# Performance work log

Hardware: AMD Instinct MI355X
Metric: run time of the kernel (lower is better)

The kernel has to match this reference:

```python
import jax, jax.numpy as jnp
import numpy as np
import math

B, S, D_MODEL, H, D_LATENT = 2, 2048, 2048, 16, 512
D_HEAD = D_MODEL // H


def setup_inputs() -> dict:
    key = jax.random.key(0)
    ks = jax.random.split(key, 6)
    s = lambda fan: 1.0 / math.sqrt(fan)
    return {
        "x": jax.random.normal(ks[0], (B, S, D_MODEL), dtype=jnp.float32),
        "W_q": jax.random.normal(ks[1], (D_MODEL, D_MODEL), dtype=jnp.float32) * s(D_MODEL),
        "W_down_kv": jax.random.normal(ks[2], (D_LATENT, D_MODEL), dtype=jnp.float32) * s(D_MODEL),
        "W_up_k": jax.random.normal(ks[3], (H, D_HEAD, D_LATENT), dtype=jnp.float32) * s(D_LATENT),
        "W_up_v": jax.random.normal(ks[4], (H, D_HEAD, D_LATENT), dtype=jnp.float32) * s(D_LATENT),
        "W_o": jax.random.normal(ks[5], (D_MODEL, D_MODEL), dtype=jnp.float32) * s(D_MODEL),
    }


def reference(x, W_q, W_down_kv, W_up_k, W_up_v, W_o):
    b, s_len, d_model = x.shape
    # Q: (B, H, S, Dh)
    Q = (x @ W_q.T).reshape(b, s_len, H, D_HEAD).transpose(0, 2, 1, 3)
    # latent KV: (B, S, d_latent)
    C_kv = x @ W_down_kv.T
    # per-head up-projections fused into one einsum: (B, H, S, Dh)
    K = jnp.einsum("bsl,hdl->bhsd", C_kv, W_up_k)
    V = jnp.einsum("bsl,hdl->bhsd", C_kv, W_up_v)
    scores = jnp.einsum("bhsd,bhtd->bhst", Q, K) / math.sqrt(D_HEAD)
    attn = jax.nn.softmax(scores, axis=-1)  # dropout p=0 / eval -> identity
    out = jnp.einsum("bhst,bhtd->bhsd", attn, V)
    out = out.transpose(0, 2, 1, 3).reshape(b, s_len, H * D_HEAD)
    return out @ W_o.T
```

## Files before the change

kernel.cpp:

```cpp
#include <hip/hip_runtime.h>
#include <hip/hip_bf16.h>

typedef __hip_bfloat16 bf16;
typedef __attribute__((ext_vector_type(8))) short short8v;
typedef __attribute__((ext_vector_type(4))) short short4v;
typedef __attribute__((ext_vector_type(4))) float f32x4;
typedef __attribute__((ext_vector_type(16))) float f32x16;
typedef __attribute__((ext_vector_type(4))) unsigned int uint4v;
typedef unsigned int u32;

#define MFMA_16x16x32(a, b, c) __builtin_amdgcn_mfma_f32_16x16x32_bf16((a), (b), (c), 0, 0, 0)
#define MFMA_32x32x16(a, b, c) __builtin_amdgcn_mfma_f32_32x32x16_bf16((a), (b), (c), 0, 0, 0)

constexpr int Bc = 2, Sc = 2048, DMc = 2048, Hc = 16, DLc = 512, DHc = 128;

__device__ __forceinline__ void gload_lds16(const bf16* g, void* lds) {
  __builtin_amdgcn_global_load_lds(
      (const __attribute__((address_space(1))) void*)g,
      (__attribute__((address_space(3))) void*)lds, 16, 0, 0);
}

__device__ __forceinline__ unsigned short bf16bits(float f) {
  return __builtin_bit_cast(unsigned short, __float2bfloat16(f));
}

struct CvtArgs {
  const float* src[6];
  bf16* dst[6];
  unsigned int cum[6];
  unsigned int total4;
};

__global__ __launch_bounds__(256) void cvt_all_kernel(CvtArgs a)
{
  unsigned int i = blockIdx.x * 256 + threadIdx.x;
  const unsigned int stride = gridDim.x * 256;
  for (; i < a.total4; i += stride) {
    int s = 0;
#pragma unroll
    for (int k = 1; k < 6; ++k) s += (i >= a.cum[k]) ? 1 : 0;
    unsigned int off = (i - a.cum[s]) * 4;
    float4 v = *(const float4*)(a.src[s] + off);
    short4v p;
    p[0] = (short)bf16bits(v.x);
    p[1] = (short)bf16bits(v.y);
    p[2] = (short)bf16bits(v.z);
    p[3] = (short)bf16bits(v.w);
    *(short4v*)(a.dst[s] + off) = p;
  }
}

template<int EPI>
__device__ __forceinline__ void gemm_tile_128(
    const bf16* __restrict__ A, const bf16* __restrict__ BT, void* __restrict__ Cv,
    int K, int ldc, int row0, int col0, bf16* As, bf16* Bs)
{
  const int tid = threadIdx.x;
  const int lane = tid & 63, wid = tid >> 6;
  const int wr = wid >> 1, wc = wid & 1;

  f32x4 acc[4][4] = {};

  const int srow = tid >> 2;
  const int scol = (tid & 3) * 8;
  const bf16* Ag = A + (size_t)(row0 + srow) * K + scol;
  const bf16* Bg = BT + (size_t)(col0 + srow) * K + scol;
  char* AsW = (char*)As + wid * 1024;
  char* BsW = (char*)Bs + wid * 1024;

  const int fr = lane & 15, fk = (lane >> 4) * 8;
  const bf16* aRd = As + (wr * 64 + fr) * 32 + fk;
  const bf16* bRd = Bs + (wc * 64 + fr) * 32 + fk;

  for (int k0 = 0; k0 < K; k0 += 32) {
    gload_lds16(Ag, AsW);
    gload_lds16(Ag + (size_t)64 * K, AsW + 4096);
    gload_lds16(Bg, BsW);
    gload_lds16(Bg + (size_t)64 * K, BsW + 4096);
    Ag += 32; Bg += 32;
    __syncthreads();
    short8v a[4], b[4];
#pragma unroll
    for (int m = 0; m < 4; ++m) a[m] = *(const short8v*)(aRd + m * 16 * 32);
#pragma unroll
    for (int n = 0; n < 4; ++n) b[n] = *(const short8v*)(bRd + n * 16 * 32);
#pragma unroll
    for (int m = 0; m < 4; ++m)
#pragma unroll
      for (int n = 0; n < 4; ++n)
        acc[m][n] = MFMA_16x16x32(a[m], b[n], acc[m][n]);
    __syncthreads();
  }

  const int crow = (lane >> 4) * 4, ccol = lane & 15;
  if (EPI == 0) {
    bf16* C = (bf16*)Cv;
#pragma unroll
    for (int m = 0; m < 4; ++m)
#pragma unroll
      for (int n = 0; n < 4; ++n) {
        bf16* Cp = C + (size_t)(row0 + wr * 64 + m * 16 + crow) * ldc
                     + col0 + wc * 64 + n * 16 + ccol;
#pragma unroll
        for (int r = 0; r < 4; ++r)
          Cp[(size_t)r * ldc] = __float2bfloat16(acc[m][n][r]);
      }
  } else if (EPI == 1) {
    bf16* C = (bf16*)Cv;
#pragma unroll
    for (int m = 0; m < 4; ++m)
#pragma unroll
      for (int n = 0; n < 4; ++n) {
        short4v pk;
#pragma unroll
        for (int r = 0; r < 4; ++r)
          pk[r] = (short)bf16bits(acc[m][n][r]);
        bf16* Cp = C + (size_t)(col0 + wc * 64 + n * 16 + ccol) * ldc
                     + row0 + wr * 64 + m * 16 + crow;
        *(short4v*)Cp = pk;
      }
  } else {
    float* C = (float*)Cv;
#pragma unroll
    for (int m = 0; m < 4; ++m)
#pragma unroll
      for (int n = 0; n < 4; ++n) {
        float* Cp = C + (size_t)(row0 + wr * 64 + m * 16 + crow) * ldc
                      + col0 + wc * 64 + n * 16 + ccol;
#pragma unroll
        for (int r = 0; r < 4; ++r)
          Cp[(size_t)r * ldc] = acc[m][n][r];
      }
  }
}

__device__ __forceinline__ int2 xcd_remap(int nx, int ny) {
  int flat = blockIdx.x + nx * blockIdx.y;
  int chunk = (nx * ny) >> 3;
  int role = (flat & 7) * chunk + (flat >> 3);
  return make_int2(role % nx, role / nx);
}

template<int EPI>
__global__ __launch_bounds__(256) void gemm_bt_kernel(
    const bf16* __restrict__ A, const bf16* __restrict__ BT, void* __restrict__ C,
    int K, int N)
{
  __shared__ bf16 As[128 * 32];
  __shared__ bf16 Bs[128 * 32];
  int2 bb = xcd_remap(gridDim.x, gridDim.y);
  gemm_tile_128<EPI>(A, BT, C, K, N, bb.y * 128, bb.x * 128, As, Bs);
}

__global__ __launch_bounds__(256) void qkv_gemm_kernel(
    const bf16* __restrict__ xb, const bf16* __restrict__ Wqb,
    const bf16* __restrict__ Wdkvb, bf16* __restrict__ Qb, bf16* __restrict__ Ck)
{
  __shared__ bf16 As[128 * 32];
  __shared__ bf16 Bs[128 * 32];
  int2 bb = xcd_remap(20, 32);
  const int bx = bb.x, row0 = bb.y * 128;
  if (bx < 16)
    gemm_tile_128<0>(xb, Wqb, Qb, DMc, DMc, row0, bx * 128, As, Bs);
  else
    gemm_tile_128<0>(xb, Wdkvb, Ck, DMc, DLc, row0, (bx - 16) * 128, As, Bs);
}

#define GPHASE(bufv, KK, MH)                                                \
  do {                                                                      \
    const char* ap_ = aR + (bufv) * 32768 + (KK) * 8192 + (MH) * 4096;      \
    const char* bp_ = bR + (bufv) * 32768 + (KK) * 8192;                    \
    short8v af_[4], bf_[4];                                                 \
    _Pragma("unroll")                                                       \
    for (int m4 = 0; m4 < 4; ++m4)                                          \
      af_[m4] = *(const short8v*)(ap_ + m4 * 1024);                         \
    _Pragma("unroll")                                                       \
    for (int n = 0; n < 4; ++n)                                             \
      bf_[n] = *(const short8v*)(bp_ + n * 1024);                           \
    __builtin_amdgcn_s_setprio(1);                                          \
    _Pragma("unroll")                                                       \
    for (int m4 = 0; m4 < 4; ++m4)                                          \
      _Pragma("unroll")                                                     \
      for (int n = 0; n < 4; ++n)                                           \
        acc[(MH) * 4 + m4][n] =                                             \
            MFMA_16x16x32(af_[m4], bf_[n], acc[(MH) * 4 + m4][n]);          \
    __builtin_amdgcn_s_setprio(0);                                          \
  } while (0)

template<int EPI>
__device__ __forceinline__ void gemm_tile_256(
    const bf16* __restrict__ A, const bf16* __restrict__ BT, void* __restrict__ Cv,
    int K, int ldc, int row0, int col0, char* AsC, char* BsC)
{
  const int tid = threadIdx.x;
  const int lane = tid & 63, wid = tid >> 6;
  const int wm = wid >> 2, wn = wid & 3;
  const int fr = lane & 15, g = lane >> 4;

  f32x4 acc[8][4] = {};

  const int srow = tid >> 2;
  const int scolS = ((tid & 3) * 16) ^ (((srow >> 1) & 3) << 4);
  const bf16* sA = A + (size_t)(row0 + srow) * K + (scolS >> 1);
  const bf16* sB = BT + (size_t)(col0 + srow) * K + (scolS >> 1);
  char* AsW = AsC + wid * 1024;
  char* BsW = BsC + wid * 1024;

  auto ISSA = [&](int buf, int h, int kk, int kt) {
    gload_lds16(sA + (size_t)(h * 128) * K + kt * 64 + kk * 32,
                AsW + buf * 32768 + h * 16384 + kk * 8192);
  };
  auto ISSB = [&](int buf, int h, int kk, int kt) {
    gload_lds16(sB + (size_t)(h * 128) * K + kt * 64 + kk * 32,
                BsW + buf * 32768 + h * 16384 + kk * 8192);
  };

  const int rdLane = fr * 64 + ((g * 16) ^ (((fr >> 1) & 3) << 4));
  const char* aR = AsC + wm * 16384 + rdLane;
  const char* bR = BsC + (wn >> 1) * 16384 + (wn & 1) * 4096 + rdLane;

  ISSA(0, 0, 0, 0); ISSA(0, 1, 0, 0); ISSB(0, 0, 0, 0); ISSB(0, 1, 0, 0);
  ISSA(0, 0, 1, 0); ISSA(0, 1, 1, 0); ISSB(0, 0, 1, 0); ISSB(0, 1, 1, 0);

  const int KT = K >> 6;
  for (int kt = 0; kt < KT - 1; ++kt) {
    const int buf = kt & 1, nb = buf ^ 1;
    asm volatile("s_waitcnt vmcnt(4)" ::: "memory");
    __builtin_amdgcn_s_barrier();
    asm volatile("" ::: "memory");
    ISSA(nb, 0, 0, kt + 1); ISSA(nb, 1, 0, kt + 1);
    GPHASE(buf, 0, 0);
    ISSB(nb, 0, 0, kt + 1); ISSB(nb, 1, 0, kt + 1);
    GPHASE(buf, 0, 1);
    asm volatile("s_waitcnt vmcnt(4)" ::: "memory");
    __builtin_amdgcn_s_barrier();
    asm volatile("" ::: "memory");
    ISSA(nb, 0, 1, kt + 1); ISSA(nb, 1, 1, kt + 1);
    GPHASE(buf, 1, 0);
    ISSB(nb, 0, 1, kt + 1); ISSB(nb, 1, 1, kt + 1);
    GPHASE(buf, 1, 1);
  }
  {
    const int buf = (KT - 1) & 1;
    asm volatile("s_waitcnt vmcnt(4)" ::: "memory");
    __builtin_amdgcn_s_barrier();
    asm volatile("" ::: "memory");
    GPHASE(buf, 0, 0);
    GPHASE(buf, 0, 1);
    asm volatile("s_waitcnt vmcnt(0)" ::: "memory");
    __builtin_amdgcn_s_barrier();
    asm volatile("" ::: "memory");
    GPHASE(buf, 1, 0);
    GPHASE(buf, 1, 1);
  }

  const int crow = g * 4, ccol = fr;
  if (EPI == 0) {
    bf16* C = (bf16*)Cv;
#pragma unroll
    for (int m = 0; m < 8; ++m)
#pragma unroll
      for (int n = 0; n < 4; ++n) {
        bf16* Cp = C + (size_t)(row0 + wm * 128 + m * 16 + crow) * ldc
                     + col0 + wn * 64 + n * 16 + ccol;
#pragma unroll
        for (int r = 0; r < 4; ++r)
          Cp[(size_t)r * ldc] = __float2bfloat16(acc[m][n][r]);
      }
  } else if (EPI == 1) {
    bf16* C = (bf16*)Cv;
#pragma unroll
    for (int m = 0; m < 8; ++m)
#pragma unroll
      for (int n = 0; n < 4; ++n) {
        short4v pk;
#pragma unroll
        for (int r = 0; r < 4; ++r)
          pk[r] = (short)bf16bits(acc[m][n][r]);
        bf16* Cp = C + (size_t)(col0 + wn * 64 + n * 16 + ccol) * ldc
                     + row0 + wm * 128 + m * 16 + crow;
        *(short4v*)Cp = pk;
      }
  } else {
    float* C = (float*)Cv;
#pragma unroll
    for (int m = 0; m < 8; ++m)
#pragma unroll
      for (int n = 0; n < 4; ++n) {
        float* Cp = C + (size_t)(row0 + wm * 128 + m * 16 + crow) * ldc
                      + col0 + wn * 64 + n * 16 + ccol;
#pragma unroll
        for (int r = 0; r < 4; ++r)
          Cp[(size_t)r * ldc] = acc[m][n][r];
      }
  }
}

__global__ __launch_bounds__(512, 2) void up_gemm_kernel(
    const bf16* __restrict__ Ck, const bf16* __restrict__ Wukb,
    const bf16* __restrict__ Wuvb, bf16* __restrict__ Kcat, bf16* __restrict__ VTcat)
{
  __shared__ char As[65536];
  __shared__ char Bs[65536];
  const int flat = blockIdx.x + 16 * blockIdx.y;
  const int role = (flat & 7) * 32 + (flat >> 3);
  const int bx = role & 15, by = role >> 4;
  if (bx < 8)
    gemm_tile_256<0>(Ck, Wukb, Kcat, DLc, DMc, by * 256, bx * 256, As, Bs);
  else
    gemm_tile_256<1>(Ck, Wuvb, VTcat, DLc, Bc * Sc, by * 256, (bx - 8) * 256, As, Bs);
}

constexpr int KVB = 64;
constexpr int NTT = Sc / KVB;
constexpr int VSTR = Bc * Sc;

__global__ __launch_bounds__(256, 2) void mla_attn_kernel(
    const bf16* __restrict__ Q, const bf16* __restrict__ Kcat,
    const bf16* __restrict__ VTcat, bf16* __restrict__ O)
{
  __shared__ bf16 Ks[2][KVB * 128];
  __shared__ bf16 Vs[2][64 * 128];

  const int tid = threadIdx.x, lane = tid & 63, wid = tid >> 6;
  const int l31 = lane & 31, hi = lane >> 5;

  const int flat = blockIdx.x + 16 * (blockIdx.y + 16 * blockIdx.z);
  const int role = (flat & 7) * 64 + (flat >> 3);
  const int qb = role & 15, h = (role >> 4) & 15, b = role >> 8;
  const int q0 = qb * 128 + wid * 32;

  const bf16* Qp = Q + (size_t)(b * Sc + q0 + l31) * DMc + h * DHc + hi * 8;
  short8v qf[8];
#pragma unroll
  for (int kk = 0; kk < 8; ++kk) qf[kk] = *(const short8v*)(Qp + kk * 16);

  const bf16* Kb = Kcat + (size_t)b * Sc * DMc + h * DHc;
  const bf16* Vb = VTcat + (size_t)(h * DHc) * VSTR + b * Sc;

  const int srow = wid * 4 + (lane >> 4);
  const int scolB = (lane & 15) * 16;
  const int swzK0 = ((srow & 7) << 4) ^ (((srow >> 3) & 1) << 6);
  const bf16* kpE = Kb + (size_t)srow * DMc + (((scolB ^ swzK0) & 255) >> 1);
  const bf16* kpO = Kb + (size_t)srow * DMc + ((((scolB ^ swzK0) ^ 128) & 255) >> 1);
  const int swzV0 = ((srow & 7) << 4) ^ (((srow >> 3) & 1) << 7);
  const int vcp = scolB ^ swzV0;
  const bf16* vp = Vb + (size_t)(2 * srow + (vcp >> 7)) * VSTR + ((vcp & 127) >> 1);

  auto STAGE = [&](int buf, int t0) {
    char* kd = (char*)(&Ks[buf][0]) + wid * 1024;
    gload_lds16(kpE + (size_t)t0 * DMc, kd);
    gload_lds16(kpO + (size_t)(t0 + 16) * DMc, kd + 4096);
    gload_lds16(kpE + (size_t)(t0 + 32) * DMc, kd + 8192);
    gload_lds16(kpO + (size_t)(t0 + 48) * DMc, kd + 12288);
    char* vd = (char*)(&Vs[buf][0]) + wid * 1024;
    const bf16* v0 = vp + t0;
    gload_lds16(v0, vd);
    gload_lds16(v0 + (size_t)32 * VSTR, vd + 4096);
    gload_lds16(v0 + (size_t)64 * VSTR, vd + 8192);
    gload_lds16(v0 + (size_t)96 * VSTR, vd + 12288);
  };

  const int swzR = ((l31 & 7) << 4) ^ (((l31 >> 3) & 1) << 6) ^ (((l31 >> 4) & 1) << 7);
  const int swzVR = (((l31 >> 1) & 7) << 4) ^ (((l31 >> 4) & 1) << 7);

  f32x16 oacc[4] = {};
  float m_r = -1e30f, l_r = 0.f, msc = 0.f;
  const float SCL2 = 0.12751650f;
  const float THRraw = 47.0f;

  STAGE(0, 0);
  int cur = 0;

  for (int it = 0; it < NTT; ++it) {
    asm volatile("s_waitcnt vmcnt(0)" ::: "memory");
    __builtin_amdgcn_s_barrier();
    asm volatile("" ::: "memory");
    if (it + 1 < NTT) STAGE(cur ^ 1, (it + 1) * KVB);
    asm volatile("" ::: "memory");

    f32x16 s0 = {}, s1 = {};
    const char* Kc = (const char*)(&Ks[cur][0]);
    __builtin_amdgcn_s_setprio(1);
#pragma unroll
    for (int kk = 0; kk < 8; ++kk) {
      const int cb = (kk * 32 + hi * 16) ^ swzR;
      short8v k0 = *(const short8v*)(Kc + l31 * 256 + cb);
      short8v k1 = *(const short8v*)(Kc + (32 + l31) * 256 + cb);
      s0 = MFMA_32x32x16(k0, qf[kk], s0);
      s1 = MFMA_32x32x16(k1, qf[kk], s1);
    }
    __builtin_amdgcn_s_setprio(0);

    float pm = s0[0];
#pragma unroll
    for (int i = 1; i < 16; ++i) pm = fmaxf(pm, s0[i]);
#pragma unroll
    for (int i = 0; i < 16; ++i) pm = fmaxf(pm, s1[i]);

    if (!__all(pm - m_r <= THRraw)) {
      float red = fmaxf(pm, __shfl_xor(pm, 32, 64));
      float mnew = fmaxf(m_r, red);
      float c = exp2f((m_r - mnew) * SCL2);
      m_r = mnew;
      msc = mnew * SCL2;
      l_r *= c;
#pragma unroll
      for (int db = 0; db < 4; ++db) oacc[db] *= c;
    }

    short8v pf[4];
#pragma unroll
    for (int tt = 0; tt < 2; ++tt) {
      const f32x16& s = tt ? s1 : s0;
#pragma unroll
      for (int half = 0; half < 2; ++half) {
        float e0 = exp2f(__builtin_fmaf(s[half * 8 + 0], SCL2, -msc));
        float e1 = exp2f(__builtin_fmaf(s[half * 8 + 1], SCL2, -msc));
        float e2 = exp2f(__builtin_fmaf(s[half * 8 + 2], SCL2, -msc));
        float e3 = exp2f(__builtin_fmaf(s[half * 8 + 3], SCL2, -msc));
        float e4 = exp2f(__builtin_fmaf(s[half * 8 + 4], SCL2, -msc));
        float e5 = exp2f(__builtin_fmaf(s[half * 8 + 5], SCL2, -msc));
        float e6 = exp2f(__builtin_fmaf(s[half * 8 + 6], SCL2, -msc));
        float e7 = exp2f(__builtin_fmaf(s[half * 8 + 7], SCL2, -msc));
        l_r += ((e0 + e1) + (e2 + e3)) + ((e4 + e5) + (e6 + e7));
        u32 cA, cB, cC, cD;
        asm("v_cvt_pk_bf16_f32 %0, %1, %2" : "=v"(cA) : "v"(e0), "v"(e1));
        asm("v_cvt_pk_bf16_f32 %0, %1, %2" : "=v"(cB) : "v"(e2), "v"(e3));
        asm("v_cvt_pk_bf16_f32 %0, %1, %2" : "=v"(cC) : "v"(e4), "v"(e5));
        asm("v_cvt_pk_bf16_f32 %0, %1, %2" : "=v"(cD) : "v"(e6), "v"(e7));
        asm volatile("v_permlane32_swap_b32 %0, %1" : "+v"(cA), "+v"(cC));
        asm volatile("v_permlane32_swap_b32 %0, %1" : "+v"(cB), "+v"(cD));
        uint4v w;
        w[0] = cA; w[1] = cB; w[2] = cC; w[3] = cD;
        pf[tt * 2 + half] = __builtin_bit_cast(short8v, w);
      }
    }

    const char* Vc = (const char*)(&Vs[cur][0]);
    __builtin_amdgcn_s_setprio(1);
#pragma unroll
    for (int db = 0; db < 4; ++db) {
      const int vrow = (db * 16 + (l31 >> 1)) * 256;
#pragma unroll
      for (int ts = 0; ts < 4; ++ts) {
        const int cb = ((l31 & 1) * 128 + ts * 32 + hi * 16) ^ swzVR;
        short8v vf = *(const short8v*)(Vc + vrow + cb);
        oacc[db] = MFMA_32x32x16(vf, pf[ts], oacc[db]);
      }
    }
    __builtin_amdgcn_s_setprio(0);

    cur ^= 1;
  }

  float l = l_r + __shfl_xor(l_r, 32, 64);
  float inv = 1.f / l;
  bf16* Op = O + (size_t)(b * Sc + q0 + l31) * DMc + h * DHc + hi * 4;
#pragma unroll
  for (int db = 0; db < 4; ++db) {
#pragma unroll
    for (int rq = 0; rq < 4; ++rq) {
      short4v pk;
#pragma unroll
      for (int r = 0; r < 4; ++r)
        pk[r] = (short)bf16bits(oacc[db][rq * 4 + r] * inv);
      *(short4v*)(Op + db * 32 + rq * 8) = pk;
    }
  }
}

extern "C" void kernel_launch(void* const* d_in, const int* in_sizes, int n_in,
                              void* d_out, int out_size, void* d_ws, size_t ws_size,
                              hipStream_t stream)
{
  const float* x    = (const float*)d_in[0];
  const float* Wq   = (const float*)d_in[1];
  const float* Wdkv = (const float*)d_in[2];
  const float* Wuk  = (const float*)d_in[3];
  const float* Wuv  = (const float*)d_in[4];
  const float* Wo   = (const float*)d_in[5];
  float* out = (float*)d_out;

  char* ws = (char*)d_ws;
  bf16* Qb    = (bf16*)(ws + 0);
  bf16* Kcat  = (bf16*)(ws + 16777216);
  bf16* VTcat = (bf16*)(ws + 33554432);
  bf16* xb    = (bf16*)(ws + 50331648);
  bf16* AO    = (bf16*)(ws + 50331648);
  bf16* Ck    = (bf16*)(ws + 67108864);
  bf16* Wqb   = (bf16*)(ws + 71303168);
  bf16* Wdkvb = (bf16*)(ws + 79691776);
  bf16* Wukb  = (bf16*)(ws + 81788928);
  bf16* Wuvb  = (bf16*)(ws + 83886080);
  bf16* Wob   = (bf16*)(ws + 85983232);

  dim3 blk(256, 1, 1);

  CvtArgs ca;
  ca.src[0] = x;    ca.dst[0] = xb;
  ca.src[1] = Wq;   ca.dst[1] = Wqb;
  ca.src[2] = Wdkv; ca.dst[2] = Wdkvb;
  ca.src[3] = Wuk;  ca.dst[3] = Wukb;
  ca.src[4] = Wuv;  ca.dst[4] = Wuvb;
  ca.src[5] = Wo;   ca.dst[5] = Wob;
  unsigned int n4[6] = { (unsigned)(Bc * Sc * DMc / 4), (unsigned)(DMc * DMc / 4),
                         (unsigned)(DLc * DMc / 4),     (unsigned)(Hc * DHc * DLc / 4),
                         (unsigned)(Hc * DHc * DLc / 4),(unsigned)(DMc * DMc / 4) };
  unsigned int acc = 0;
  for (int i = 0; i < 6; ++i) { ca.cum[i] = acc; acc += n4[i]; }
  ca.total4 = acc;
  cvt_all_kernel<<<2048, blk, 0, stream>>>(ca);

  qkv_gemm_kernel<<<dim3(20, 32), blk, 0, stream>>>(xb, Wqb, Wdkvb, Qb, Ck);

  up_gemm_kernel<<<dim3(16, 16), dim3(512, 1, 1), 0, stream>>>(Ck, Wukb, Wuvb, Kcat, VTcat);

  mla_attn_kernel<<<dim3(Sc / 128, Hc, Bc), dim3(256, 1, 1), 0, stream>>>(
      Qb, Kcat, VTcat, AO);

  gemm_bt_kernel<2><<<dim3(16, 32), blk, 0, stream>>>(AO, Wob, out, DMc, DMc);
}
```

Baseline: 235.5 us.

## Software-pipeline attention loop so QK of next tile overlaps softmax of current

```diff
diff --git a/kernel.cpp b/kernel.cpp
--- a/kernel.cpp
+++ b/kernel.cpp
@@ -365,94 +365,124 @@
   const int swzVR = (((l31 >> 1) & 7) << 4) ^ (((l31 >> 4) & 1) << 7);
 
   f32x16 oacc[4] = {};
+  f32x16 sA0, sA1, sB0, sB1;
+  short8v pf[4];
   float m_r = -1e30f, l_r = 0.f, msc = 0.f;
   const float SCL2 = 0.12751650f;
   const float THRraw = 47.0f;
 
+#define QK_STEP(BC, S0, S1)                                                 \
+  do {                                                                      \
+    const char* Kc_ = (const char*)(&Ks[BC][0]);                            \
+    __builtin_amdgcn_s_setprio(1);                                          \
+    _Pragma("unroll")                                                       \
+    for (int kk = 0; kk < 8; ++kk) {                                        \
+      const int cb_ = (kk * 32 + hi * 16) ^ swzR;                           \
+      short8v k0_ = *(const short8v*)(Kc_ + l31 * 256 + cb_);               \
+      short8v k1_ = *(const short8v*)(Kc_ + (32 + l31) * 256 + cb_);        \
+      S0 = MFMA_32x32x16(k0_, qf[kk], S0);                                  \
+      S1 = MFMA_32x32x16(k1_, qf[kk], S1);                                  \
+    }                                                                       \
+    __builtin_amdgcn_s_setprio(0);                                          \
+  } while (0)
+
+#define SOFTMAX(S0, S1)                                                     \
+  do {                                                                      \
+    float pm = (S0)[0];                                                     \
+    _Pragma("unroll")                                                       \
+    for (int i = 1; i < 16; ++i) pm = fmaxf(pm, (S0)[i]);                   \
+    _Pragma("unroll")                                                       \
+    for (int i = 0; i < 16; ++i) pm = fmaxf(pm, (S1)[i]);                   \
+    if (!__all(pm - m_r <= THRraw)) {                                       \
+      float red = fmaxf(pm, __shfl_xor(pm, 32, 64));                        \
+      float mnew = fmaxf(m_r, red);                                         \
+      float c = exp2f((m_r - mnew) * SCL2);                                 \
+      m_r = mnew;                                                           \
+      msc = mnew * SCL2;                                                    \
+      l_r *= c;                                                             \
+      _Pragma("unroll")                                                     \
+      for (int db = 0; db < 4; ++db) oacc[db] *= c;                         \
+    }                                                                       \
+    _Pragma("unroll")                                                       \
+    for (int tt = 0; tt < 2; ++tt) {                                        \
+      const f32x16& s_ = tt ? (S1) : (S0);                                  \
+      _Pragma("unroll")                                                     \
+      for (int half = 0; half < 2; ++half) {                                \
+        float e0 = exp2f(__builtin_fmaf(s_[half * 8 + 0], SCL2, -msc));     \
+        float e1 = exp2f(__builtin_fmaf(s_[half * 8 + 1], SCL2, -msc));     \
+        float e2 = exp2f(__builtin_fmaf(s_[half * 8 + 2], SCL2, -msc));     \
+        float e3 = exp2f(__builtin_fmaf(s_[half * 8 + 3], SCL2, -msc));     \
+        float e4 = exp2f(__builtin_fmaf(s_[half * 8 + 4], SCL2, -msc));     \
+        float e5 = exp2f(__builtin_fmaf(s_[half * 8 + 5], SCL2, -msc));     \
+        float e6 = exp2f(__builtin_fmaf(s_[half * 8 + 6], SCL2, -msc));     \
+        float e7 = exp2f(__builtin_fmaf(s_[half * 8 + 7], SCL2, -msc));     \
+        l_r += ((e0 + e1) + (e2 + e3)) + ((e4 + e5) + (e6 + e7));           \
+        u32 cA, cB, cC, cD;                                                 \
+        asm("v_cvt_pk_bf16_f32 %0, %1, %2" : "=v"(cA) : "v"(e0), "v"(e1));  \
+        asm("v_cvt_pk_bf16_f32 %0, %1, %2" : "=v"(cB) : "v"(e2), "v"(e3));  \
+        asm("v_cvt_pk_bf16_f32 %0, %1, %2" : "=v"(cC) : "v"(e4), "v"(e5));  \
+        asm("v_cvt_pk_bf16_f32 %0, %1, %2" : "=v"(cD) : "v"(e6), "v"(e7));  \
+        asm volatile("v_permlane32_swap_b32 %0, %1" : "+v"(cA), "+v"(cC));  \
+        asm volatile("v_permlane32_swap_b32 %0, %1" : "+v"(cB), "+v"(cD));  \
+        uint4v w;                                                           \
+        w[0] = cA; w[1] = cB; w[2] = cC; w[3] = cD;                         \
+        pf[tt * 2 + half] = __builtin_bit_cast(short8v, w);                 \
+      }                                                                     \
+    }                                                                       \
+  } while (0)
+
+#define PV_STEP(BC)                                                         \
+  do {                                                                      \
+    const char* Vc_ = (const char*)(&Vs[BC][0]);                            \
+    __builtin_amdgcn_s_setprio(1);                                          \
+    _Pragma("unroll")                                                       \
+    for (int db = 0; db < 4; ++db) {                                        \
+      const int vrow_ = (db * 16 + (l31 >> 1)) * 256;                       \
+      _Pragma("unroll")                                                     \
+      for (int ts = 0; ts < 4; ++ts) {                                      \
+        const int cb_ = ((l31 & 1) * 128 + ts * 32 + hi * 16) ^ swzVR;      \
+        short8v vf_ = *(const short8v*)(Vc_ + vrow_ + cb_);                 \
+        oacc[db] = MFMA_32x32x16(vf_, pf[ts], oacc[db]);                    \
+      }                                                                     \
+    }                                                                       \
+    __builtin_amdgcn_s_setprio(0);                                          \
+  } while (0)
+
+#define AITER(IT, SO0, SO1, SN0, SN1, DOSTAGE)                              \
+  do {                                                                      \
+    asm volatile("s_waitcnt vmcnt(0)" ::: "memory");                        \
+    __builtin_amdgcn_s_barrier();                                           \
+    asm volatile("" ::: "memory");                                          \
+    SN0 = (f32x16){}; SN1 = (f32x16){};                                     \
+    QK_STEP((IT) & 1, SN0, SN1);                                            \
+    SOFTMAX(SO0, SO1);                                                      \
+    PV_STEP(((IT) - 1) & 1);                                                \
+    __builtin_amdgcn_s_barrier();                                           \
+    asm volatile("" ::: "memory");                                          \
+    if (DOSTAGE) STAGE(((IT) + 1) & 1, ((IT) + 1) * KVB);                   \
+    asm volatile("" ::: "memory");                                          \
+  } while (0)
+
   STAGE(0, 0);
-  int cur = 0;
-
-  for (int it = 0; it < NTT; ++it) {
-    asm volatile("s_waitcnt vmcnt(0)" ::: "memory");
-    __builtin_amdgcn_s_barrier();
-    asm volatile("" ::: "memory");
-    if (it + 1 < NTT) STAGE(cur ^ 1, (it + 1) * KVB);
-    asm volatile("" ::: "memory");
-
-    f32x16 s0 = {}, s1 = {};
-    const char* Kc = (const char*)(&Ks[cur][0]);
-    __builtin_amdgcn_s_setprio(1);
-#pragma unroll
-    for (int kk = 0; kk < 8; ++kk) {
-      const int cb = (kk * 32 + hi * 16) ^ swzR;
-      short8v k0 = *(const short8v*)(Kc + l31 * 256 + cb);
-      short8v k1 = *(const short8v*)(Kc + (32 + l31) * 256 + cb);
-      s0 = MFMA_32x32x16(k0, qf[kk], s0);
-      s1 = MFMA_32x32x16(k1, qf[kk], s1);
-    }
-    __builtin_amdgcn_s_setprio(0);
-
-    float pm = s0[0];
-#pragma unroll
-    for (int i = 1; i < 16; ++i) pm = fmaxf(pm, s0[i]);
-#pragma unroll
-    for (int i = 0; i < 16; ++i) pm = fmaxf(pm, s1[i]);
-
-    if (!__all(pm - m_r <= THRraw)) {
-      float red = fmaxf(pm, __shfl_xor(pm, 32, 64));
-      float mnew = fmaxf(m_r, red);
-      float c = exp2f((m_r - mnew) * SCL2);
-      m_r = mnew;
-      msc = mnew * SCL2;
-      l_r *= c;
-#pragma unroll
-      for (int db = 0; db < 4; ++db) oacc[db] *= c;
-    }
-
-    short8v pf[4];
-#pragma unroll
-    for (int tt = 0; tt < 2; ++tt) {
-      const f32x16& s = tt ? s1 : s0;
-#pragma unroll
-      for (int half = 0; half < 2; ++half) {
-        float e0 = exp2f(__builtin_fmaf(s[half * 8 + 0], SCL2, -msc));
-        float e1 = exp2f(__builtin_fmaf(s[half * 8 + 1], SCL2, -msc));
-        float e2 = exp2f(__builtin_fmaf(s[half * 8 + 2], SCL2, -msc));
-        float e3 = exp2f(__builtin_fmaf(s[half * 8 + 3], SCL2, -msc));
-        float e4 = exp2f(__builtin_fmaf(s[half * 8 + 4], SCL2, -msc));
-        float e5 = exp2f(__builtin_fmaf(s[half * 8 + 5], SCL2, -msc));
-        float e6 = exp2f(__builtin_fmaf(s[half * 8 + 6], SCL2, -msc));
-        float e7 = exp2f(__builtin_fmaf(s[half * 8 + 7], SCL2, -msc));
-        l_r += ((e0 + e1) + (e2 + e3)) + ((e4 + e5) + (e6 + e7));
-        u32 cA, cB, cC, cD;
-        asm("v_cvt_pk_bf16_f32 %0, %1, %2" : "=v"(cA) : "v"(e0), "v"(e1));
-        asm("v_cvt_pk_bf16_f32 %0, %1, %2" : "=v"(cB) : "v"(e2), "v"(e3));
-        asm("v_cvt_pk_bf16_f32 %0, %1, %2" : "=v"(cC) : "v"(e4), "v"(e5));
-        asm("v_cvt_pk_bf16_f32 %0, %1, %2" : "=v"(cD) : "v"(e6), "v"(e7));
-        asm volatile("v_permlane32_swap_b32 %0, %1" : "+v"(cA), "+v"(cC));
-        asm volatile("v_permlane32_swap_b32 %0, %1" : "+v"(cB), "+v"(cD));
-        uint4v w;
-        w[0] = cA; w[1] = cB; w[2] = cC; w[3] = cD;
-        pf[tt * 2 + half] = __builtin_bit_cast(short8v, w);
-      }
-    }
-
-    const char* Vc = (const char*)(&Vs[cur][0]);
-    __builtin_amdgcn_s_setprio(1);
-#pragma unroll
-    for (int db = 0; db < 4; ++db) {
-      const int vrow = (db * 16 + (l31 >> 1)) * 256;
-#pragma unroll
-      for (int ts = 0; ts < 4; ++ts) {
-        const int cb = ((l31 & 1) * 128 + ts * 32 + hi * 16) ^ swzVR;
-        short8v vf = *(const short8v*)(Vc + vrow + cb);
-        oacc[db] = MFMA_32x32x16(vf, pf[ts], oacc[db]);
-      }
-    }
-    __builtin_amdgcn_s_setprio(0);
-
-    cur ^= 1;
-  }
+  asm volatile("s_waitcnt vmcnt(0)" ::: "memory");
+  __builtin_amdgcn_s_barrier();
+  asm volatile("" ::: "memory");
+  STAGE(1, KVB);
+  sA0 = (f32x16){}; sA1 = (f32x16){};
+  QK_STEP(0, sA0, sA1);
+
+  for (int p = 0; p < 15; ++p) {
+    AITER(2 * p + 1, sA0, sA1, sB0, sB1, 1);
+    AITER(2 * p + 2, sB0, sB1, sA0, sA1, 1);
+  }
+  AITER(31, sA0, sA1, sB0, sB1, 0);
+  SOFTMAX(sB0, sB1);
+  PV_STEP(1);
+
+#undef AITER
+#undef PV_STEP
+#undef SOFTMAX
+#undef QK_STEP
 
   float l = l_r + __shfl_xor(l_r, 32, 64);
   float inv = 1.f / l;
```

Measured after the change: 236.7 us. No clear change (+0.5%).
